# Kernel optimization log

Hardware: AMD Instinct MI355X
Metric: run time of the kernel (lower is better)

The kernel has to match this reference:

```python
import jax, jax.numpy as jnp
import numpy as np

EMBED_DIM = 1024
N_HEADS = 16
HEAD_DIM = EMBED_DIM // N_HEADS
MAX_REL_POS = 2  # hardcoded in the torch module


def _rel_index(length_q, length_k):
    # final_mat[i, j] = clip(i - j, -p, p) + p  with i over k-range, j over q-range
    rq = jnp.arange(length_q)[None, :]
    rk = jnp.arange(length_k)[:, None]
    dist = jnp.clip(rk - rq, -MAX_REL_POS, MAX_REL_POS) + MAX_REL_POS
    return dist  # (len_k, len_q) int; square when len_q == len_k


def setup_inputs() -> dict:
    key = jax.random.key(0)
    ks = jax.random.split(key, 16)
    B, S, E, H, D = 4, 1024, EMBED_DIM, N_HEADS, HEAD_DIM
    xavier = lambda k, shape: jax.random.uniform(
        k, shape, jnp.float32, -1.0, 1.0) * np.sqrt(6.0 / (shape[0] + shape[1]))
    return {
        "query": jax.random.normal(ks[0], (B, S, E), jnp.float32),
        "key": jax.random.normal(ks[1], (B, S, E), jnp.float32),
        "value": jax.random.normal(ks[2], (B, S, E), jnp.float32),
        "Wq": xavier(ks[3], (E, E)), "bq": jnp.zeros((E,), jnp.float32),
        "Wk": xavier(ks[4], (E, E)), "bk": jnp.zeros((E,), jnp.float32),
        "Wv": xavier(ks[5], (E, E)), "bv": jnp.zeros((E,), jnp.float32),
        "Wo": xavier(ks[6], (E, E)), "bo": jnp.zeros((E,), jnp.float32),
        "rpk_table": xavier(ks[7], (2 * MAX_REL_POS + 1, D)),
        "rpv_table": xavier(ks[8], (2 * MAX_REL_POS + 1, D)),
    }


def reference(query, key, value, Wq, bq, Wk, bk, Wv, bv, Wo, bo, rpk_table, rpv_table):
    B, S, E = query.shape
    H, D = N_HEADS, HEAD_DIM
    q = query @ Wq.T + bq
    _k = key @ Wk.T + bk      # computed but unused (faithful to source bug)
    v = value @ Wv.T + bv

    qh = q.reshape(B, S, H, D).transpose(0, 2, 1, 3)   # b h s d
    vh = v.reshape(B, S, H, D).transpose(0, 2, 1, 3)

    # NOTE: source uses query for both sides of the dot product
    dots = jnp.einsum('bhqd,bhkd->bhqk', qh, qh)

    idx = _rel_index(S, S)                              # (S, S)
    rpk = rpk_table[idx]                                # (S, S, D)
    rp_dots = jnp.einsum('bhqd,qkd->bhqk', qh, rpk)

    scale = jnp.sqrt(jnp.asarray(D, q.dtype))
    attn = jax.nn.softmax((dots + rp_dots) / scale, axis=-1)

    weight1 = jnp.einsum('bhqk,bhkd->bhqd', attn, vh)
    rpv = rpv_table[idx]                                # (S, S, D)
    weight2 = jnp.einsum('bhqk,qkd->bhqd', attn, rpv)

    out = (weight1 + weight2).transpose(0, 2, 1, 3).reshape(B, S, E)
    return out @ Wo.T + bo
```

## Files before the change

kernel.cpp:

```cpp
#include <hip/hip_runtime.h>


typedef _Float16 v8h __attribute__((ext_vector_type(8)));
typedef _Float16 v4h __attribute__((ext_vector_type(4)));
typedef _Float16 v2h __attribute__((ext_vector_type(2)));
typedef float    v4f __attribute__((ext_vector_type(4)));

#define MFMA_F16(A_, B_, C_) __builtin_amdgcn_mfma_f32_16x16x32_f16(A_, B_, C_, 0, 0, 0)

__device__ __forceinline__ void async_copy16(const void* g, void* l) {
    __builtin_amdgcn_global_load_lds(
        (const __attribute__((address_space(1))) void*)g,
        (__attribute__((address_space(3))) void*)l, 16, 0, 0);
}

__global__ __launch_bounds__(256) void cvt5_kernel(
    const float* __restrict__ s0, const float* __restrict__ s1,
    const float* __restrict__ s2, const float* __restrict__ s3,
    const float* __restrict__ s4,
    _Float16* __restrict__ d0, _Float16* __restrict__ d1,
    _Float16* __restrict__ d2, _Float16* __restrict__ d3,
    _Float16* __restrict__ d4,
    int n0, int n1, int n2, int n3, int n4)
{
    const float* s; _Float16* d; int n;
    switch (blockIdx.y) {
        case 0:  s = s0; d = d0; n = n0; break;
        case 1:  s = s1; d = d1; n = n1; break;
        case 2:  s = s2; d = d2; n = n2; break;
        case 3:  s = s3; d = d3; n = n3; break;
        default: s = s4; d = d4; n = n4; break;
    }
    int i = (blockIdx.x * 256 + threadIdx.x) * 4;
    if (i >= n) return;
    float4 f = *(const float4*)(s + i);
    v4h o = { (_Float16)f.x, (_Float16)f.y, (_Float16)f.z, (_Float16)f.w };
    *(v4h*)(d + i) = o;
}

template<int TM>
__device__ __forceinline__ void gemm_core(const _Float16* __restrict__ A,
                                          const _Float16* __restrict__ W,
                                          const float* __restrict__ bias,
                                          int mode, void* __restrict__ outp)
{
    __shared__ __align__(16) _Float16 smem[2 * 128 * 64];
    _Float16* As = smem;
    _Float16* Bs = smem + 128 * 64;

    const int tid  = threadIdx.x;
    const int wave = tid >> 6, lane = tid & 63;
    const int quad = lane >> 4, n16 = lane & 15;
    const int wm = (TM == 128) ? (wave >> 1) : 0;
    const int wn = (TM == 128) ? (wave & 1) : wave;
    const int WCOLS = (TM == 128) ? 64 : 32;
    const int NJ = WCOLS / 16;
    const int row0 = blockIdx.y * TM, col0 = blockIdx.x * 128;
    const int rL = lane >> 3, c8 = lane & 7;
    const int lcs = c8 ^ rL;

    v4f acc[4][4] = {};

    for (int kb = 0; kb < 1024; kb += 64) {
        __syncthreads();
        #pragma unroll
        for (int p = 0; p < TM / 32; p++) {
            int rg = wave * (TM / 32) + p;
            int row = rg * 8 + rL;
            async_copy16(A + (size_t)(row0 + row) * 1024 + kb + lcs * 8, &As[rg * 512]);
        }
        #pragma unroll
        for (int p = 0; p < 4; p++) {
            int rg = wave * 4 + p;
            int row = rg * 8 + rL;
            async_copy16(W + (size_t)(col0 + row) * 1024 + kb + lcs * 8, &Bs[rg * 512]);
        }
        __syncthreads();
        #pragma unroll
        for (int ks = 0; ks < 64; ks += 32) {
            const int pc = ((ks >> 3) + quad) ^ (n16 & 7);
            v8h af[4], bf[4];
            #pragma unroll
            for (int i = 0; i < 4; i++)
                af[i] = *(const v8h*)(&As[(wm * 64 + i * 16 + n16) * 64 + pc * 8]);
            #pragma unroll
            for (int j = 0; j < NJ; j++)
                bf[j] = *(const v8h*)(&Bs[(wn * WCOLS + j * 16 + n16) * 64 + pc * 8]);
            #pragma unroll
            for (int i = 0; i < 4; i++)
                #pragma unroll
                for (int j = 0; j < NJ; j++)
                    acc[i][j] = MFMA_F16(af[i], bf[j], acc[i][j]);
        }
    }

    __syncthreads();
    char* scb = (char*)smem + wave * 8192;

    const int b     = (row0 + wm * 64) >> 10;
    const int srow0 = (row0 + wm * 64) & 1023;

    if (mode == 0) {
        _Float16* sc = (_Float16*)scb;
        #pragma unroll
        for (int i = 0; i < 4; i++)
            #pragma unroll
            for (int j = 0; j < 4; j++)
                #pragma unroll
                for (int r = 0; r < 4; r++) {
                    int rowL = i * 16 + quad * 4 + r, colL = j * 16 + n16;
                    float v = acc[i][j][r] + bias[col0 + wn * 64 + colL];
                    sc[rowL * 64 + (((colL >> 3) ^ (rowL & 7)) << 3) + (colL & 7)] = (_Float16)v;
                }
        int h = (col0 + wn * 64) >> 6;
        #pragma unroll
        for (int it = 0; it < 8; it++) {
            int rowR = it * 8 + (lane >> 3), cR = lane & 7;
            v8h val = *(const v8h*)(&sc[rowR * 64 + ((cR ^ (rowR & 7)) << 3)]);
            *(v8h*)((_Float16*)outp +
                    (((size_t)(b * 16 + h) * 1024 + srow0 + rowR) << 6) + cR * 8) = val;
        }
    } else if (mode == 1) {
        _Float16* sc = (_Float16*)scb;
        #pragma unroll
        for (int i = 0; i < 4; i++)
            #pragma unroll
            for (int j = 0; j < 4; j++) {
                int colL = j * 16 + n16;
                int c16 = i * 2 + (quad >> 1);
                v4h pk;
                #pragma unroll
                for (int r = 0; r < 4; r++)
                    pk[r] = (_Float16)(acc[i][j][r] + bias[col0 + wn * 64 + colL]);
                *(v4h*)(&sc[colL * 64 + ((c16 ^ (colL & 7)) << 3) + (quad & 1) * 4]) = pk;
            }
        #pragma unroll
        for (int it = 0; it < 8; it++) {
            int dR = it * 8 + (lane >> 3), scn = lane & 7;
            v8h val = *(const v8h*)(&sc[dR * 64 + ((scn ^ (dR & 7)) << 3)]);
            int cg = col0 + wn * 64 + dR;
            int h = cg >> 6, dl = cg & 63;
            *(v8h*)((_Float16*)outp +
                    ((size_t)((b * 16 + h) * 64 + dl) << 10) + srow0 + scn * 8) = val;
        }
    } else {
        float* sc = (float*)scb;
        #pragma unroll
        for (int i = 0; i < 4; i++)
            #pragma unroll
            for (int j = 0; j < 2; j++)
                #pragma unroll
                for (int r = 0; r < 4; r++) {
                    int rowL = i * 16 + quad * 4 + r, colL = j * 16 + n16;
                    sc[rowL * 32 + (((colL >> 2) ^ (rowL & 7)) << 2) + (colL & 3)] =
                        acc[i][j][r] + bias[col0 + wn * 32 + colL];
                }
        #pragma unroll
        for (int it = 0; it < 8; it++) {
            int rowR = it * 8 + (lane >> 3), cR = lane & 7;
            v4f val = *(const v4f*)(&sc[rowR * 32 + ((cR ^ (rowR & 7)) << 2)]);
            *(v4f*)((float*)outp + (size_t)(row0 + rowR) * 1024 + col0 + wn * 32 + cR * 4) = val;
        }
    }
}

__global__ __launch_bounds__(256) void gemm_qv_kernel(
    const _Float16* __restrict__ Aq, const _Float16* __restrict__ Av,
    const _Float16* __restrict__ Wq, const _Float16* __restrict__ Wv,
    const float* __restrict__ bq, const float* __restrict__ bv,
    _Float16* __restrict__ q_out, _Float16* __restrict__ v_out)
{
    int z = blockIdx.z;
    gemm_core<128>(z ? Av : Aq, z ? Wv : Wq, z ? bv : bq, z ? 1 : 0,
                   z ? (void*)v_out : (void*)q_out);
}

__global__ __launch_bounds__(256) void gemm_o_kernel(
    const _Float16* __restrict__ A, const _Float16* __restrict__ W,
    const float* __restrict__ bias, float* __restrict__ outp)
{
    gemm_core<64>(A, W, bias, 2, (void*)outp);
}

__global__ __launch_bounds__(256) void attn_kernel(
    const _Float16* __restrict__ qb,
    const _Float16* __restrict__ vt,
    const float* __restrict__ rpk, const float* __restrict__ rpv,
    _Float16* __restrict__ attn_o)
{
    const int blk = blockIdx.x;
    const int bh = blk & 63;
    const int q0 = (blk >> 6) * 64;
    const int tid = threadIdx.x;
    const int wave = tid >> 6, lane = tid & 63;
    const int quad = lane >> 4, n16 = lane & 15;
    const int qw = q0 + wave * 16;
    const _Float16* Qh = qb + (size_t)bh * 1024 * 64;
    const _Float16* Vh = vt + (size_t)bh * 64 * 1024;

    __shared__ __align__(16) _Float16 Ks[2][64 * 64];
    __shared__ __align__(16) _Float16 Vs[2][64 * 64];
    __shared__ float rqs[4][16][5];

    const int rL = lane >> 3, c8 = lane & 7;
    const int lcs = c8 ^ rL;

    {
        #pragma unroll
        for (int p = 0; p < 2; p++) {
            int c = wave * 2 + p;
            int row = c * 8 + rL;
            async_copy16(Qh + (size_t)row * 64 + lcs * 8, &Ks[0][c * 512]);
            async_copy16(Vh + (size_t)row * 1024 + lcs * 8, &Vs[0][c * 512]);
        }
    }

    {
        int m = lane >> 2, seg = lane & 3;
        const _Float16* qrow = Qh + (size_t)(qw + m) * 64 + seg * 16;
        v8h qa = *(const v8h*)(qrow);
        v8h qc = *(const v8h*)(qrow + 8);
        float qd[16];
        #pragma unroll
        for (int x = 0; x < 8; x++) { qd[x] = (float)qa[x]; qd[8 + x] = (float)qc[x]; }
        float qq = 0.f;
        #pragma unroll
        for (int x = 0; x < 16; x++) qq += qd[x] * qd[x];
        qq += __shfl_xor(qq, 1);
        qq += __shfl_xor(qq, 2);
        #pragma unroll
        for (int t = 0; t < 5; t++) {
            float s = 0.f;
            #pragma unroll
            for (int x = 0; x < 16; x++) s += qd[x] * rpk[t * 64 + seg * 16 + x];
            s += __shfl_xor(s, 1);
            s += __shfl_xor(s, 2);
            if (seg == 0) rqs[wave][m][t] = (s - qq) * 0.125f;
        }
    }

    v8h aq0 = *(const v8h*)(Qh + (size_t)(qw + n16) * 64 + quad * 8);
    v8h aq1 = *(const v8h*)(Qh + (size_t)(qw + n16) * 64 + 32 + quad * 8);

    __syncthreads();

    float rc[5];
    #pragma unroll
    for (int t = 0; t < 5; t++) rc[t] = rqs[wave][n16][t];

    float bkt[5] = {0.f, 0.f, 0.f, 0.f, 0.f};
    v4f O[4] = {};

    const int pphys0 = quad ^ (n16 & 7);
    const int pphys1 = (quad + 4) ^ (n16 & 7);
    const int srcA = ((quad & 1) << 5) + n16;
    const int srcB = srcA + 16;
    const bool tHi = (quad >> 1) != 0;

    for (int it = 0; it < 16; ++it) {
        const int cur = it & 1;
        const int kb = it * 64;
        if (it + 1 < 16) {
            const int nxt = 1 - cur;
            const int kn = kb + 64;
            #pragma unroll
            for (int p = 0; p < 2; p++) {
                int c = wave * 2 + p;
                int row = c * 8 + rL;
                async_copy16(Qh + (size_t)(kn + row) * 64 + lcs * 8, &Ks[nxt][c * 512]);
                async_copy16(Vh + (size_t)row * 1024 + kn + lcs * 8, &Vs[nxt][c * 512]);
            }
        }

        int pkLo[4], pkHi[4];
        #pragma unroll
        for (int t = 0; t < 4; t++) {
            v8h ak0 = *(const v8h*)(&Ks[cur][(t * 16 + n16) * 64 + pphys0 * 8]);
            v8h ak1 = *(const v8h*)(&Ks[cur][(t * 16 + n16) * 64 + pphys1 * 8]);
            v4f s = {0.f, 0.f, 0.f, 0.f};
            s = MFMA_F16(ak0, aq0, s);
            s = MFMA_F16(ak1, aq1, s);
            const int dqt = qw - kb - t * 16;
            float pv[4];
            if (dqt >= 32) {
                #pragma unroll
                for (int r = 0; r < 4; r++) {
                    float p = __expf(fmaf(s[r], 0.125f, rc[4]));
                    pv[r] = p; bkt[4] += p;
                }
            } else if (dqt <= -32) {
                #pragma unroll
                for (int r = 0; r < 4; r++) {
                    float p = __expf(fmaf(s[r], 0.125f, rc[0]));
                    pv[r] = p; bkt[0] += p;
                }
            } else {
                #pragma unroll
                for (int r = 0; r < 4; r++) {
                    int diff = dqt + n16 - quad * 4 - r;
                    float rv = diff >= 2  ? rc[4]
                             : diff == 1  ? rc[3]
                             : diff == 0  ? rc[2]
                             : diff == -1 ? rc[1]
                                          : rc[0];
                    float p = __expf(fmaf(s[r], 0.125f, rv));
                    pv[r] = p;
                    bkt[4] += (diff >= 2)  ? p : 0.f;
                    bkt[3] += (diff == 1)  ? p : 0.f;
                    bkt[2] += (diff == 0)  ? p : 0.f;
                    bkt[1] += (diff == -1) ? p : 0.f;
                    bkt[0] += (diff <= -2) ? p : 0.f;
                }
            }
            pkLo[t] = __builtin_bit_cast(int, __builtin_amdgcn_cvt_pkrtz(pv[0], pv[1]));
            pkHi[t] = __builtin_bit_cast(int, __builtin_amdgcn_cvt_pkrtz(pv[2], pv[3]));
        }

        int aL0 = __shfl(pkLo[0], srcA), aH0 = __shfl(pkHi[0], srcA);
        int bL0 = __shfl(pkLo[0], srcB), bH0 = __shfl(pkHi[0], srcB);
        int aL1 = __shfl(pkLo[1], srcA), aH1 = __shfl(pkHi[1], srcA);
        int bL1 = __shfl(pkLo[1], srcB), bH1 = __shfl(pkHi[1], srcB);
        int aL2 = __shfl(pkLo[2], srcA), aH2 = __shfl(pkHi[2], srcA);
        int bL2 = __shfl(pkLo[2], srcB), bH2 = __shfl(pkHi[2], srcB);
        int aL3 = __shfl(pkLo[3], srcA), aH3 = __shfl(pkHi[3], srcA);
        int bL3 = __shfl(pkLo[3], srcB), bH3 = __shfl(pkHi[3], srcB);
        union { int d[4]; v8h v; } u0, u1;
        u0.d[0] = tHi ? aL1 : aL0;  u0.d[1] = tHi ? aH1 : aH0;
        u0.d[2] = tHi ? bL1 : bL0;  u0.d[3] = tHi ? bH1 : bH0;
        u1.d[0] = tHi ? aL3 : aL2;  u1.d[1] = tHi ? aH3 : aH2;
        u1.d[2] = tHi ? bL3 : bL2;  u1.d[3] = tHi ? bH3 : bH2;
        v8h pf0 = u0.v, pf1 = u1.v;

        #pragma unroll
        for (int dt = 0; dt < 4; dt++) {
            v8h av0 = *(const v8h*)(&Vs[cur][(dt * 16 + n16) * 64 + pphys0 * 8]);
            v8h av1 = *(const v8h*)(&Vs[cur][(dt * 16 + n16) * 64 + pphys1 * 8]);
            O[dt] = MFMA_F16(av0, pf0, O[dt]);
            O[dt] = MFMA_F16(av1, pf1, O[dt]);
        }

        __syncthreads();
    }

    #pragma unroll
    for (int t = 0; t < 5; t++) {
        bkt[t] += __shfl_xor(bkt[t], 16);
        bkt[t] += __shfl_xor(bkt[t], 32);
    }
    float l = bkt[0] + bkt[1] + bkt[2] + bkt[3] + bkt[4];
    float inv = 1.0f / l;
    int q = qw + n16;
    size_t orow = (size_t)((bh >> 4) * 1024 + q) * 1024 + (bh & 15) * 64;
    #pragma unroll
    for (int dt = 0; dt < 4; dt++) {
        int d0 = dt * 16 + quad * 4;
        v4h st;
        #pragma unroll
        for (int r = 0; r < 4; r++) {
            int d = d0 + r;
            float w2 = bkt[4] * rpv[4 * 64 + d] + bkt[3] * rpv[3 * 64 + d]
                     + bkt[2] * rpv[2 * 64 + d] + bkt[1] * rpv[1 * 64 + d]
                     + bkt[0] * rpv[0 * 64 + d];
            st[r] = (_Float16)((O[dt][r] + w2) * inv);
        }
        *(v4h*)(attn_o + orow + d0) = st;
    }
}

extern "C" void kernel_launch(void* const* d_in, const int* in_sizes, int n_in,
                              void* d_out, int out_size, void* d_ws, size_t ws_size,
                              hipStream_t stream)
{
    const float* query = (const float*)d_in[0];
    const float* value = (const float*)d_in[2];
    const float* Wq = (const float*)d_in[3];
    const float* bq = (const float*)d_in[4];
    const float* Wv = (const float*)d_in[7];
    const float* bv = (const float*)d_in[8];
    const float* Wo = (const float*)d_in[9];
    const float* bo = (const float*)d_in[10];
    const float* rpk = (const float*)d_in[11];
    const float* rpv = (const float*)d_in[12];
    float* out = (float*)d_out;

    char* ws = (char*)d_ws;
    const size_t MB = 1024 * 1024;
    _Float16* q_bhsd = (_Float16*)(ws);
    _Float16* v_t    = (_Float16*)(ws + 8 * MB);
    _Float16* q16    = (_Float16*)(ws + 16 * MB);
    _Float16* attn_o = (_Float16*)(ws + 16 * MB);
    _Float16* v16    = (_Float16*)(ws + 24 * MB);
    _Float16* wq16   = (_Float16*)(ws + 32 * MB);
    _Float16* wv16   = (_Float16*)(ws + 34 * MB);
    _Float16* wo16   = (_Float16*)(ws + 36 * MB);

    cvt5_kernel<<<dim3(4096, 5), 256, 0, stream>>>(
        query, value, Wq, Wv, Wo, q16, v16, wq16, wv16, wo16,
        4096 * 1024, 4096 * 1024, 1024 * 1024, 1024 * 1024, 1024 * 1024);

    gemm_qv_kernel<<<dim3(8, 32, 2), 256, 0, stream>>>(
        q16, v16, wq16, wv16, bq, bv, q_bhsd, v_t);

    attn_kernel<<<dim3(1024), 256, 0, stream>>>(q_bhsd, v_t, rpk, rpv, attn_o);

    gemm_o_kernel<<<dim3(8, 64), 256, 0, stream>>>(attn_o, wo16, bo, out);
}
```

Before: 209.3 us.

## Swizzle GEMM block order and pass attention probabilities through LDS

The GEMM kernels now use a 1D grid with a remapped block order. Groups of 8 consecutive blocks share a column tile and walk down rows, so weight tiles are reused while still in L2. In the attention kernel, the P-matrix register shuffle (16 shfl ops plus selects) is replaced by a per-wave LDS scratch area with an XOR swizzle. The same scratch area replaces the relative-position score array. This trades cross-lane shuffles for LDS writes and reads, which adds LDS traffic and extra ordering requirements within each wave.

```diff
diff --git a/kernel.cpp b/kernel.cpp
--- a/kernel.cpp
+++ b/kernel.cpp
@@ -3,7 +3,6 @@
 
 typedef _Float16 v8h __attribute__((ext_vector_type(8)));
 typedef _Float16 v4h __attribute__((ext_vector_type(4)));
-typedef _Float16 v2h __attribute__((ext_vector_type(2)));
 typedef float    v4f __attribute__((ext_vector_type(4)));
 
 #define MFMA_F16(A_, B_, C_) __builtin_amdgcn_mfma_f32_16x16x32_f16(A_, B_, C_, 0, 0, 0)
@@ -42,7 +41,8 @@
 __device__ __forceinline__ void gemm_core(const _Float16* __restrict__ A,
                                           const _Float16* __restrict__ W,
                                           const float* __restrict__ bias,
-                                          int mode, void* __restrict__ outp)
+                                          int mode, void* __restrict__ outp,
+                                          int row0, int col0)
 {
     __shared__ __align__(16) _Float16 smem[2 * 128 * 64];
     _Float16* As = smem;
@@ -55,7 +55,6 @@
     const int wn = (TM == 128) ? (wave & 1) : wave;
     const int WCOLS = (TM == 128) ? 64 : 32;
     const int NJ = WCOLS / 16;
-    const int row0 = blockIdx.y * TM, col0 = blockIdx.x * 128;
     const int rL = lane >> 3, c8 = lane & 7;
     const int lcs = c8 ^ rL;
 
@@ -170,16 +169,22 @@
     const float* __restrict__ bq, const float* __restrict__ bv,
     _Float16* __restrict__ q_out, _Float16* __restrict__ v_out)
 {
-    int z = blockIdx.z;
+    int id = blockIdx.x;
+    int y = (id & 7) | (((id >> 3) & 3) << 3);
+    int x = (id >> 5) & 7;
+    int z = id >> 8;
     gemm_core<128>(z ? Av : Aq, z ? Wv : Wq, z ? bv : bq, z ? 1 : 0,
-                   z ? (void*)v_out : (void*)q_out);
+                   z ? (void*)v_out : (void*)q_out, y * 128, x * 128);
 }
 
 __global__ __launch_bounds__(256) void gemm_o_kernel(
     const _Float16* __restrict__ A, const _Float16* __restrict__ W,
     const float* __restrict__ bias, float* __restrict__ outp)
 {
-    gemm_core<64>(A, W, bias, 2, (void*)outp);
+    int id = blockIdx.x;
+    int y = (id & 7) | (((id >> 3) & 7) << 3);
+    int x = id >> 6;
+    gemm_core<64>(A, W, bias, 2, (void*)outp, y * 64, x * 128);
 }
 
 __global__ __launch_bounds__(256) void attn_kernel(
@@ -200,21 +205,20 @@
 
     __shared__ __align__(16) _Float16 Ks[2][64 * 64];
     __shared__ __align__(16) _Float16 Vs[2][64 * 64];
-    __shared__ float rqs[4][16][5];
+    __shared__ __align__(16) _Float16 Ps[4][16 * 64];
 
     const int rL = lane >> 3, c8 = lane & 7;
     const int lcs = c8 ^ rL;
 
-    {
-        #pragma unroll
-        for (int p = 0; p < 2; p++) {
-            int c = wave * 2 + p;
-            int row = c * 8 + rL;
-            async_copy16(Qh + (size_t)row * 64 + lcs * 8, &Ks[0][c * 512]);
-            async_copy16(Vh + (size_t)row * 1024 + lcs * 8, &Vs[0][c * 512]);
-        }
-    }
-
+    #pragma unroll
+    for (int p = 0; p < 2; p++) {
+        int c = wave * 2 + p;
+        int row = c * 8 + rL;
+        async_copy16(Qh + (size_t)row * 64 + lcs * 8, &Ks[0][c * 512]);
+        async_copy16(Vh + (size_t)row * 1024 + lcs * 8, &Vs[0][c * 512]);
+    }
+
+    float* rqs_w = (float*)&Ps[wave][0];
     {
         int m = lane >> 2, seg = lane & 3;
         const _Float16* qrow = Qh + (size_t)(qw + m) * 64 + seg * 16;
@@ -235,7 +239,7 @@
             for (int x = 0; x < 16; x++) s += qd[x] * rpk[t * 64 + seg * 16 + x];
             s += __shfl_xor(s, 1);
             s += __shfl_xor(s, 2);
-            if (seg == 0) rqs[wave][m][t] = (s - qq) * 0.125f;
+            if (seg == 0) rqs_w[m * 5 + t] = (s - qq) * 0.125f;
         }
     }
 
@@ -246,16 +250,13 @@
 
     float rc[5];
     #pragma unroll
-    for (int t = 0; t < 5; t++) rc[t] = rqs[wave][n16][t];
+    for (int t = 0; t < 5; t++) rc[t] = rqs_w[n16 * 5 + t];
 
     float bkt[5] = {0.f, 0.f, 0.f, 0.f, 0.f};
     v4f O[4] = {};
 
     const int pphys0 = quad ^ (n16 & 7);
     const int pphys1 = (quad + 4) ^ (n16 & 7);
-    const int srcA = ((quad & 1) << 5) + n16;
-    const int srcB = srcA + 16;
-    const bool tHi = (quad >> 1) != 0;
 
     for (int it = 0; it < 16; ++it) {
         const int cur = it & 1;
@@ -272,7 +273,6 @@
             }
         }
 
-        int pkLo[4], pkHi[4];
         #pragma unroll
         for (int t = 0; t < 4; t++) {
             v8h ak0 = *(const v8h*)(&Ks[cur][(t * 16 + n16) * 64 + pphys0 * 8]);
@@ -312,25 +312,13 @@
                     bkt[0] += (diff <= -2) ? p : 0.f;
                 }
             }
-            pkLo[t] = __builtin_bit_cast(int, __builtin_amdgcn_cvt_pkrtz(pv[0], pv[1]));
-            pkHi[t] = __builtin_bit_cast(int, __builtin_amdgcn_cvt_pkrtz(pv[2], pv[3]));
-        }
-
-        int aL0 = __shfl(pkLo[0], srcA), aH0 = __shfl(pkHi[0], srcA);
-        int bL0 = __shfl(pkLo[0], srcB), bH0 = __shfl(pkHi[0], srcB);
-        int aL1 = __shfl(pkLo[1], srcA), aH1 = __shfl(pkHi[1], srcA);
-        int bL1 = __shfl(pkLo[1], srcB), bH1 = __shfl(pkHi[1], srcB);
-        int aL2 = __shfl(pkLo[2], srcA), aH2 = __shfl(pkHi[2], srcA);
-        int bL2 = __shfl(pkLo[2], srcB), bH2 = __shfl(pkHi[2], srcB);
-        int aL3 = __shfl(pkLo[3], srcA), aH3 = __shfl(pkHi[3], srcA);
-        int bL3 = __shfl(pkLo[3], srcB), bH3 = __shfl(pkHi[3], srcB);
-        union { int d[4]; v8h v; } u0, u1;
-        u0.d[0] = tHi ? aL1 : aL0;  u0.d[1] = tHi ? aH1 : aH0;
-        u0.d[2] = tHi ? bL1 : bL0;  u0.d[3] = tHi ? bH1 : bH0;
-        u1.d[0] = tHi ? aL3 : aL2;  u1.d[1] = tHi ? aH3 : aH2;
-        u1.d[2] = tHi ? bL3 : bL2;  u1.d[3] = tHi ? bH3 : bH2;
-        v8h pf0 = u0.v, pf1 = u1.v;
-
+            v4h pk = { (_Float16)pv[0], (_Float16)pv[1], (_Float16)pv[2], (_Float16)pv[3] };
+            int c16 = t * 2 + (quad >> 1);
+            *(v4h*)(&Ps[wave][n16 * 64 + ((c16 ^ (n16 & 7)) << 3) + (quad & 1) * 4]) = pk;
+        }
+
+        v8h pf0 = *(const v8h*)(&Ps[wave][n16 * 64 + pphys0 * 8]);
+        v8h pf1 = *(const v8h*)(&Ps[wave][n16 * 64 + pphys1 * 8]);
         #pragma unroll
         for (int dt = 0; dt < 4; dt++) {
             v8h av0 = *(const v8h*)(&Vs[cur][(dt * 16 + n16) * 64 + pphys0 * 8]);
@@ -398,10 +386,10 @@
         query, value, Wq, Wv, Wo, q16, v16, wq16, wv16, wo16,
         4096 * 1024, 4096 * 1024, 1024 * 1024, 1024 * 1024, 1024 * 1024);
 
-    gemm_qv_kernel<<<dim3(8, 32, 2), 256, 0, stream>>>(
+    gemm_qv_kernel<<<dim3(512), 256, 0, stream>>>(
         q16, v16, wq16, wv16, bq, bv, q_bhsd, v_t);
 
     attn_kernel<<<dim3(1024), 256, 0, stream>>>(q_bhsd, v_t, rpk, rpv, attn_o);
 
-    gemm_o_kernel<<<dim3(8, 64), 256, 0, stream>>>(attn_o, wo16, bo, out);
-}
+    gemm_o_kernel<<<dim3(512), 256, 0, stream>>>(attn_o, wo16, bo, out);
+}
```

After: 203.9 us. 1.03x faster.
